# Optimization experiments

Measured on AMD Instinct MI355X. Metric: run time of the kernel, lower is better.

The kernel has to match this reference:

```python
import jax, jax.numpy as jnp
import numpy as np
from jax import lax

B, T, D, H, O, L = 32, 2048, 256, 256, 256, 2


def setup_inputs() -> dict:
    key = jax.random.key(0)
    ks = jax.random.split(key, 16)
    s = 0.05
    inp = {"x": jax.random.normal(ks[0], (B, T, D), dtype=jnp.float32)}
    dims = [D, H]  # input dim of each layer
    for l in range(L):
        inp[f"Wi{l}"] = jax.random.normal(ks[1 + 3 * l], (dims[l], 4 * H), dtype=jnp.float32) * s
        inp[f"Wh{l}"] = jax.random.normal(ks[2 + 3 * l], (H, 4 * H), dtype=jnp.float32) * s
        inp[f"b{l}"] = jnp.zeros((4 * H,), dtype=jnp.float32)
    inp["Wd"] = jax.random.normal(ks[10], (H, O), dtype=jnp.float32) * s
    inp["bd"] = jnp.zeros((O,), dtype=jnp.float32)
    return inp


def _lstm_layer(x, Wi, Wh, b):
    # x: [B, T, Din] -> outputs h over time: [B, T, H]
    Bx = x.shape[0]
    Hh = Wh.shape[0]
    # Precompute input projections for all timesteps (one big GEMM).
    xg = jnp.einsum('btd,dg->tbg', x, Wi)  # time-major [T, B, 4H]

    def step(carry, xg_t):
        c, h = carry
        z = xg_t + h @ Wh + b  # [B, 4H]
        i, f, g, o = jnp.split(z, 4, axis=-1)  # flax gate order: i, f, g, o
        c_new = jax.nn.sigmoid(f) * c + jax.nn.sigmoid(i) * jnp.tanh(g)
        h_new = jax.nn.sigmoid(o) * jnp.tanh(c_new)
        return (c_new, h_new), h_new

    c0 = jnp.zeros((Bx, Hh), dtype=x.dtype)
    h0 = jnp.zeros((Bx, Hh), dtype=x.dtype)
    _, ys = lax.scan(step, (c0, h0), xg)  # ys: [T, B, H]
    return ys.transpose(1, 0, 2)


def reference(x, Wi0, Wh0, b0, Wi1, Wh1, b1, Wd, bd):
    y = _lstm_layer(x, Wi0, Wh0, b0)
    y = _lstm_layer(y, Wi1, Wh1, b1)
    last_hidden = y[:, -1]  # [B, H]
    return last_hidden @ Wd + bd  # [B, O]
```

## Files before the change

kernel.cpp:

```cpp
#include <hip/hip_runtime.h>
#include <stdint.h>

#define TT 2048
#define DD 256
#define GG 1024
#define HWORDS 8192
#define RING0 64
#define RING1 4
#define PROW 1024

typedef __attribute__((ext_vector_type(4))) float f32x4;
typedef __attribute__((ext_vector_type(8))) short s16x8;
typedef __attribute__((ext_vector_type(4))) unsigned u32x4;

static __device__ __forceinline__ unsigned f2bf(float f) {
    union { float f; unsigned u; } v; v.f = f;
    return (v.u + 0x7fffu + ((v.u >> 16) & 1u)) >> 16;
}
static __device__ __forceinline__ float bf2f(unsigned b) {
    union { unsigned u; float f; } v; v.u = b << 16;
    return v.f;
}
static __device__ __forceinline__ float sigm(float x) {
    return 1.0f / (1.0f + __expf(-x));
}
static __device__ __forceinline__ float tanh_f(float x) {
    x = fminf(15.0f, fmaxf(-15.0f, x));
    float e = __expf(2.0f * x);
    return (e - 1.0f) / (e + 1.0f);
}

static __device__ __forceinline__ u32x4 ld16_sys(const unsigned* p) {
    u32x4 r;
    asm volatile("global_load_dwordx4 %0, %1, off sc0 sc1"
                 : "=&v"(r) : "v"(p) : "memory");
    return r;
}
static __device__ __forceinline__ u32x4 ld16(const unsigned* p) {
    u32x4 r;
    asm volatile("global_load_dwordx4 %0, %1, off"
                 : "=&v"(r) : "v"(p) : "memory");
    return r;
}
static __device__ __forceinline__ void st4_sys(unsigned* p, unsigned d) {
    asm volatile("global_store_dword %0, %1, off sc0 sc1" :: "v"(p), "v"(d) : "memory");
}

#define VW(n) do { asm volatile("s_waitcnt vmcnt(" #n ")" ::: "memory"); \
                   __builtin_amdgcn_sched_barrier(0); } while (0)
#define LBAR() do { asm volatile("s_waitcnt lgkmcnt(0)\n\ts_barrier" ::: "memory"); \
                    __builtin_amdgcn_sched_barrier(0); } while (0)

#define KEEP8(a) asm volatile("" :: "v"(a[0]), "v"(a[1]), "v"(a[2]), "v"(a[3]), \
                                    "v"(a[4]), "v"(a[5]), "v"(a[6]), "v"(a[7]))

static __device__ __forceinline__ bool tags_ok4(const u32x4 v[8], unsigned tag) {
    unsigned d = 0;
#pragma unroll
    for (int i = 0; i < 8; ++i)
        d |= (v[i][0] ^ tag) | (v[i][1] ^ tag) | (v[i][2] ^ tag) | (v[i][3] ^ tag);
    return (d & 0xffffu) == 0;
}

__global__ void k_init(unsigned* __restrict__ h0, unsigned* __restrict__ h1) {
    unsigned i = blockIdx.x * 256 + threadIdx.x;
    h0[i] = 0u;
    if (i < RING1 * HWORDS) h1[i] = 0u;
}

__launch_bounds__(256, 1)
__global__ void k_scan(const float* __restrict__ x,
                       const float* __restrict__ Wi0, const float* __restrict__ Wh0,
                       const float* __restrict__ b0,
                       const float* __restrict__ Wi1, const float* __restrict__ Wh1,
                       const float* __restrict__ b1,
                       unsigned* h0w, unsigned* h1w)
{
    const int tid = threadIdx.x;
    const bool isL0 = (blockIdx.x < 32);
    const int w = blockIdx.x & 31;

    const float* Wi = isL0 ? Wi0 : Wi1;
    const float* Wh = isL0 ? Wh0 : Wh1;
    const float* bb = isL0 ? b0 : b1;

    __shared__ __align__(16) unsigned char Ap[32 * PROW];
    __shared__ float zbuf[4 * 32 * 10];

    const int lane = tid & 63;
    const int wid = tid >> 6;
    const int mt = wid & 1;
    const int nt = wid >> 1;

    s16x8 Bf[16];
    {
        const int jloc = lane & 15;
        const int lcol = nt * 16 + jloc;
        const int gate = lcol >> 3;
        const int jj = lcol & 7;
        const int gcol = gate * 256 + w * 8 + jj;
        const int krow = (lane >> 4) * 8;
#pragma unroll
        for (int kf = 0; kf < 16; ++kf) {
            s16x8 a;
#pragma unroll
            for (int j = 0; j < 8; ++j) {
                int k = kf * 32 + krow + j;
                float wv = (k < 256) ? Wi[(size_t)k * GG + gcol] : Wh[(size_t)(k - 256) * GG + gcol];
                a[j] = (short)f2bf(wv);
            }
            Bf[kf] = a;
        }
    }

    const int gm = tid >> 3;
    const int gj = tid & 7;
    const float bi_ = bb[0 * 256 + w * 8 + gj], bf_ = bb[1 * 256 + w * 8 + gj];
    const float bg_ = bb[2 * 256 + w * 8 + gj], bo_ = bb[3 * 256 + w * 8 + gj];

    const int cb = tid & 63;
    const int rq = tid >> 6;

    const unsigned urow = (unsigned)((tid >> 1) & 31);
    const unsigned usw = (urow & 7u) << 4;

    const unsigned arow = (unsigned)(mt * 16 + (lane & 15));
    const unsigned rb = arow * PROW;
    const unsigned asw = (arow & 7u) << 4;

    float cs = 0.f;
    long long budget = 500000;

#define UNP_STORE(A0, A1, A2, A3, BASE, I) do {                                   \
        uint2 pk_;                                                                \
        pk_.x = ((A0) >> 16) | ((A1) & 0xffff0000u);                              \
        pk_.y = ((A2) >> 16) | ((A3) & 0xffff0000u);                              \
        unsigned bcol_ = (unsigned)((I) * 4 + (tid >> 6)) * 16u                   \
                       + (unsigned)(tid & 1) * 8u;                                \
        *(uint2*)(Ap + urow * PROW + (((BASE) + bcol_) ^ usw)) = pk_;             \
    } while (0)

    if (isL0) {
        int known = 0;
        u32x4 xr[8];
#pragma unroll
        for (int i = 0; i < 8; ++i)
            xr[i] = ld16((const unsigned*)(x + (size_t)(i * 4 + rq) * (TT * DD) + cb * 4));
        VW(0);
        u32x4 pA[8] = {}, pB[8] = {};

        for (int c = 0; c < TT; ++c) {
            VW(1);
            KEEP8(pA); KEEP8(pB);
#pragma unroll
            for (int i = 0; i < 8; ++i) {
                unsigned row = (unsigned)(i * 4 + rq);
                uint2 pk;
                pk.x = f2bf(__uint_as_float(xr[i][0])) | (f2bf(__uint_as_float(xr[i][1])) << 16);
                pk.y = f2bf(__uint_as_float(xr[i][2])) | (f2bf(__uint_as_float(xr[i][3])) << 16);
                *(uint2*)(Ap + row * PROW + (((unsigned)(cb * 8)) ^ ((row & 7u) << 4))) = pk;
            }
            const unsigned* s0 = h0w + (size_t)(c & (RING0 - 1)) * HWORDS + tid * 4;
#pragma unroll
            for (int i = 0; i < 8; ++i) pA[i] = ld16_sys(s0 + i * 1024);
            LBAR();

            f32x4 acc = {0.f, 0.f, 0.f, 0.f};
#pragma unroll
            for (int kf = 0; kf < 8; ++kf) {
                unsigned kb = (unsigned)kf * 64u + ((unsigned)(lane >> 4)) * 16u;
                s16x8 a = *(const s16x8*)(Ap + rb + (kb ^ asw));
                acc = __builtin_amdgcn_mfma_f32_16x16x32_bf16(a, Bf[kf], acc, 0, 0, 0);
            }
#pragma unroll
            for (int i = 0; i < 8; ++i) pB[i] = ld16_sys(s0 + i * 1024);
            VW(8);
            bool wA = tags_ok4(pA, (unsigned)c);
            bool ok = wA;
            while (!ok) {
                if (--budget <= 0) break;
                __builtin_amdgcn_s_sleep(1);
#pragma unroll
                for (int i = 0; i < 8; ++i) pA[i] = ld16_sys(s0 + i * 1024);
                VW(8);
                if (tags_ok4(pB, (unsigned)c)) { ok = true; wA = false; break; }
                if (--budget <= 0) break;
                __builtin_amdgcn_s_sleep(1);
#pragma unroll
                for (int i = 0; i < 8; ++i) pB[i] = ld16_sys(s0 + i * 1024);
                VW(8);
                wA = tags_ok4(pA, (unsigned)c);
                ok = wA;
            }
#pragma unroll
            for (int i = 0; i < 8; ++i) {
                unsigned a0 = wA ? pA[i][0] : pB[i][0];
                unsigned a1 = wA ? pA[i][1] : pB[i][1];
                unsigned a2 = wA ? pA[i][2] : pB[i][2];
                unsigned a3 = wA ? pA[i][3] : pB[i][3];
                UNP_STORE(a0, a1, a2, a3, 512u, i);
            }
            if (c + 1 < TT) {
#pragma unroll
                for (int i = 0; i < 8; ++i)
                    xr[i] = ld16((const unsigned*)(x + (size_t)(i * 4 + rq) * (TT * DD)
                                                   + (size_t)(c + 1) * DD + cb * 4));
            }
            LBAR();

#pragma unroll
            for (int kf = 8; kf < 16; ++kf) {
                unsigned kb = (unsigned)kf * 64u + ((unsigned)(lane >> 4)) * 16u;
                s16x8 a = *(const s16x8*)(Ap + rb + (kb ^ asw));
                acc = __builtin_amdgcn_mfma_f32_16x16x32_bf16(a, Bf[kf], acc, 0, 0, 0);
            }
            {
                const int n = nt * 16 + (lane & 15);
                const int g = n >> 3, cl = n & 7;
#pragma unroll
                for (int r = 0; r < 4; ++r)
                    zbuf[g * 320 + (mt * 16 + (lane >> 4) * 4 + r) * 10 + cl] = acc[r];
            }
            LBAR();

            float zi = zbuf[0 * 320 + gm * 10 + gj] + bi_;
            float zf = zbuf[1 * 320 + gm * 10 + gj] + bf_;
            float zg = zbuf[2 * 320 + gm * 10 + gj] + bg_;
            float zo = zbuf[3 * 320 + gm * 10 + gj] + bo_;
            cs = sigm(zf) * cs + sigm(zi) * tanh_f(zg);
            float h = sigm(zo) * tanh_f(cs);

            int T = c - 63;
            if (T > known) {
                const unsigned* trow = h1w + (size_t)(T & (RING1 - 1)) * HWORDS
                                     + (size_t)(lane & 31) * 256;
                for (;;) {
                    u32x4 tv = ld16_sys(trow);
                    VW(0);
                    int m = (int)(tv[0] & 0xffffu);
                    m = min(m, (int)(tv[1] & 0xffffu));
                    m = min(m, (int)(tv[2] & 0xffffu));
                    m = min(m, (int)(tv[3] & 0xffffu));
#pragma unroll
                    for (int off = 32; off; off >>= 1) m = min(m, __shfl_xor(m, off, 64));
                    if (m >= T) { known = m; break; }
                    if (--budget <= 0) break;
                    __builtin_amdgcn_s_sleep(4);
                }
            }
            st4_sys(h0w + (size_t)((c + 1) & (RING0 - 1)) * HWORDS + w * 256 + tid,
                    (f2bf(h) << 16) | (unsigned)(c + 1));
        }
    } else {
        u32x4 ph[8], qA[8] = {}, qB[8] = {};
        {
            const unsigned* sp = h0w + (size_t)1 * HWORDS + tid * 4;
#pragma unroll
            for (int i = 0; i < 8; ++i) ph[i] = ld16_sys(sp + i * 1024);
        }
        for (int c = 0; c < TT; ++c) {
            if (c == 0) { VW(0); } else { VW(1); }
            KEEP8(qA); KEEP8(qB);
            const unsigned* s0 = h0w + (size_t)((c + 1) & (RING0 - 1)) * HWORDS + tid * 4;
            while (!tags_ok4(ph, (unsigned)(c + 1))) {
                if (--budget <= 0) break;
                __builtin_amdgcn_s_sleep(1);
#pragma unroll
                for (int i = 0; i < 8; ++i) ph[i] = ld16_sys(s0 + i * 1024);
                VW(0);
            }
#pragma unroll
            for (int i = 0; i < 8; ++i)
                UNP_STORE(ph[i][0], ph[i][1], ph[i][2], ph[i][3], 0u, i);

            const unsigned* s1 = h1w + (size_t)(c & (RING1 - 1)) * HWORDS + tid * 4;
#pragma unroll
            for (int i = 0; i < 8; ++i) qA[i] = ld16_sys(s1 + i * 1024);
            LBAR();

            f32x4 acc = {0.f, 0.f, 0.f, 0.f};
#pragma unroll
            for (int kf = 0; kf < 8; ++kf) {
                unsigned kb = (unsigned)kf * 64u + ((unsigned)(lane >> 4)) * 16u;
                s16x8 a = *(const s16x8*)(Ap + rb + (kb ^ asw));
                acc = __builtin_amdgcn_mfma_f32_16x16x32_bf16(a, Bf[kf], acc, 0, 0, 0);
            }
#pragma unroll
            for (int i = 0; i < 8; ++i) qB[i] = ld16_sys(s1 + i * 1024);
            VW(8);
            bool wA = tags_ok4(qA, (unsigned)c);
            bool ok = wA;
            while (!ok) {
                if (--budget <= 0) break;
                __builtin_amdgcn_s_sleep(1);
#pragma unroll
                for (int i = 0; i < 8; ++i) qA[i] = ld16_sys(s1 + i * 1024);
                VW(8);
                if (tags_ok4(qB, (unsigned)c)) { ok = true; wA = false; break; }
                if (--budget <= 0) break;
                __builtin_amdgcn_s_sleep(1);
#pragma unroll
                for (int i = 0; i < 8; ++i) qB[i] = ld16_sys(s1 + i * 1024);
                VW(8);
                wA = tags_ok4(qA, (unsigned)c);
                ok = wA;
            }
#pragma unroll
            for (int i = 0; i < 8; ++i) {
                unsigned a0 = wA ? qA[i][0] : qB[i][0];
                unsigned a1 = wA ? qA[i][1] : qB[i][1];
                unsigned a2 = wA ? qA[i][2] : qB[i][2];
                unsigned a3 = wA ? qA[i][3] : qB[i][3];
                UNP_STORE(a0, a1, a2, a3, 512u, i);
            }
            LBAR();

#pragma unroll
            for (int kf = 8; kf < 16; ++kf) {
                unsigned kb = (unsigned)kf * 64u + ((unsigned)(lane >> 4)) * 16u;
                s16x8 a = *(const s16x8*)(Ap + rb + (kb ^ asw));
                acc = __builtin_amdgcn_mfma_f32_16x16x32_bf16(a, Bf[kf], acc, 0, 0, 0);
            }
            {
                const int n = nt * 16 + (lane & 15);
                const int g = n >> 3, cl = n & 7;
#pragma unroll
                for (int r = 0; r < 4; ++r)
                    zbuf[g * 320 + (mt * 16 + (lane >> 4) * 4 + r) * 10 + cl] = acc[r];
            }
            LBAR();

            float zi = zbuf[0 * 320 + gm * 10 + gj] + bi_;
            float zf = zbuf[1 * 320 + gm * 10 + gj] + bf_;
            float zg = zbuf[2 * 320 + gm * 10 + gj] + bg_;
            float zo = zbuf[3 * 320 + gm * 10 + gj] + bo_;
            cs = sigm(zf) * cs + sigm(zi) * tanh_f(zg);
            float h = sigm(zo) * tanh_f(cs);

            if (c + 1 < TT) {
                const unsigned* sn = h0w + (size_t)((c + 2) & (RING0 - 1)) * HWORDS + tid * 4;
#pragma unroll
                for (int i = 0; i < 8; ++i) ph[i] = ld16_sys(sn + i * 1024);
            }
            st4_sys(h1w + (size_t)((c + 1) & (RING1 - 1)) * HWORDS + w * 256 + tid,
                    (f2bf(h) << 16) | (unsigned)(c + 1));
        }
    }
#undef UNP_STORE
}

__global__ void k_dense(const unsigned* __restrict__ h1last,
                        const float* __restrict__ Wd, const float* __restrict__ bd,
                        float* __restrict__ out)
{
    __shared__ float hs[256];
    const int m = blockIdx.x;
    const int o = threadIdx.x;
    hs[o] = bf2f(h1last[(o >> 3) * 256 + m * 8 + (o & 7)] >> 16);
    __syncthreads();
    float acc = bd[o];
#pragma unroll 8
    for (int k = 0; k < 256; ++k)
        acc = fmaf(hs[k], Wd[k * 256 + o], acc);
    out[m * 256 + o] = acc;
}

extern "C" void kernel_launch(void* const* d_in, const int* in_sizes, int n_in,
                              void* d_out, int out_size, void* d_ws, size_t ws_size,
                              hipStream_t stream)
{
    const float* x   = (const float*)d_in[0];
    const float* Wi0 = (const float*)d_in[1];
    const float* Wh0 = (const float*)d_in[2];
    const float* b0  = (const float*)d_in[3];
    const float* Wi1 = (const float*)d_in[4];
    const float* Wh1 = (const float*)d_in[5];
    const float* b1  = (const float*)d_in[6];
    const float* Wd  = (const float*)d_in[7];
    const float* bd  = (const float*)d_in[8];
    float* out = (float*)d_out;

    char* ws = (char*)d_ws;
    unsigned* h0w = (unsigned*)ws;
    unsigned* h1w = (unsigned*)(ws + (size_t)RING0 * HWORDS * 4);

    k_init<<<dim3(RING0 * HWORDS / 256), dim3(256), 0, stream>>>(h0w, h1w);
    k_scan<<<dim3(64), dim3(256), 0, stream>>>(x, Wi0, Wh0, b0, Wi1, Wh1, b1, h0w, h1w);
    k_dense<<<dim3(32), dim3(256), 0, stream>>>(
        h1w + (size_t)(TT & (RING1 - 1)) * HWORDS, Wd, bd, out);
}
```

Baseline: 4.634 ms.

## Restructure recurrent step: issue h polls right after publish, single barrier before MFMA

Replaces the double-buffered pA/pB speculative polling, and the split of the MFMA across two barrier phases, with one poll that is issued right after this block publishes its own h. The next step then only waits and retries before staging both halves into LDS behind a single barrier. The K loop runs as two independent accumulator chains that are summed at the end, which shortens the MFMA dependency chain. The x bf16 conversion is hoisted to the end of the previous step. The risk is that the first poll now often reads stale tags (issued immediately after the store) and needs a sleep-and-retry round trip. It also loses the overlap of the first half of the MFMA with the poll latency.

```diff
diff --git a/kernel.cpp b/kernel.cpp
--- a/kernel.cpp
+++ b/kernel.cpp
@@ -50,9 +50,6 @@
                    __builtin_amdgcn_sched_barrier(0); } while (0)
 #define LBAR() do { asm volatile("s_waitcnt lgkmcnt(0)\n\ts_barrier" ::: "memory"); \
                     __builtin_amdgcn_sched_barrier(0); } while (0)
-
-#define KEEP8(a) asm volatile("" :: "v"(a[0]), "v"(a[1]), "v"(a[2]), "v"(a[3]), \
-                                    "v"(a[4]), "v"(a[5]), "v"(a[6]), "v"(a[7]))
 
 static __device__ __forceinline__ bool tags_ok4(const u32x4 v[8], unsigned tag) {
     unsigned d = 0;
@@ -143,63 +140,41 @@
     if (isL0) {
         int known = 0;
         u32x4 xr[8];
+        uint2 cvt[8];
+        u32x4 pA[8];
 #pragma unroll
         for (int i = 0; i < 8; ++i)
             xr[i] = ld16((const unsigned*)(x + (size_t)(i * 4 + rq) * (TT * DD) + cb * 4));
         VW(0);
-        u32x4 pA[8] = {}, pB[8] = {};
+#pragma unroll
+        for (int i = 0; i < 8; ++i) {
+            cvt[i].x = f2bf(__uint_as_float(xr[i][0])) | (f2bf(__uint_as_float(xr[i][1])) << 16);
+            cvt[i].y = f2bf(__uint_as_float(xr[i][2])) | (f2bf(__uint_as_float(xr[i][3])) << 16);
+        }
+        {
+            const unsigned* s0 = h0w + tid * 4;
+#pragma unroll
+            for (int i = 0; i < 8; ++i) pA[i] = ld16_sys(s0 + i * 1024);
+        }
 
         for (int c = 0; c < TT; ++c) {
-            VW(1);
-            KEEP8(pA); KEEP8(pB);
+            const unsigned* s0 = h0w + (size_t)(c & (RING0 - 1)) * HWORDS + tid * 4;
+            VW(0);
+            while (!tags_ok4(pA, (unsigned)c)) {
+                if (--budget <= 0) break;
+                __builtin_amdgcn_s_sleep(1);
+#pragma unroll
+                for (int i = 0; i < 8; ++i) pA[i] = ld16_sys(s0 + i * 1024);
+                VW(0);
+            }
 #pragma unroll
             for (int i = 0; i < 8; ++i) {
                 unsigned row = (unsigned)(i * 4 + rq);
-                uint2 pk;
-                pk.x = f2bf(__uint_as_float(xr[i][0])) | (f2bf(__uint_as_float(xr[i][1])) << 16);
-                pk.y = f2bf(__uint_as_float(xr[i][2])) | (f2bf(__uint_as_float(xr[i][3])) << 16);
-                *(uint2*)(Ap + row * PROW + (((unsigned)(cb * 8)) ^ ((row & 7u) << 4))) = pk;
-            }
-            const unsigned* s0 = h0w + (size_t)(c & (RING0 - 1)) * HWORDS + tid * 4;
-#pragma unroll
-            for (int i = 0; i < 8; ++i) pA[i] = ld16_sys(s0 + i * 1024);
-            LBAR();
-
-            f32x4 acc = {0.f, 0.f, 0.f, 0.f};
-#pragma unroll
-            for (int kf = 0; kf < 8; ++kf) {
-                unsigned kb = (unsigned)kf * 64u + ((unsigned)(lane >> 4)) * 16u;
-                s16x8 a = *(const s16x8*)(Ap + rb + (kb ^ asw));
-                acc = __builtin_amdgcn_mfma_f32_16x16x32_bf16(a, Bf[kf], acc, 0, 0, 0);
-            }
-#pragma unroll
-            for (int i = 0; i < 8; ++i) pB[i] = ld16_sys(s0 + i * 1024);
-            VW(8);
-            bool wA = tags_ok4(pA, (unsigned)c);
-            bool ok = wA;
-            while (!ok) {
-                if (--budget <= 0) break;
-                __builtin_amdgcn_s_sleep(1);
-#pragma unroll
-                for (int i = 0; i < 8; ++i) pA[i] = ld16_sys(s0 + i * 1024);
-                VW(8);
-                if (tags_ok4(pB, (unsigned)c)) { ok = true; wA = false; break; }
-                if (--budget <= 0) break;
-                __builtin_amdgcn_s_sleep(1);
-#pragma unroll
-                for (int i = 0; i < 8; ++i) pB[i] = ld16_sys(s0 + i * 1024);
-                VW(8);
-                wA = tags_ok4(pA, (unsigned)c);
-                ok = wA;
-            }
-#pragma unroll
-            for (int i = 0; i < 8; ++i) {
-                unsigned a0 = wA ? pA[i][0] : pB[i][0];
-                unsigned a1 = wA ? pA[i][1] : pB[i][1];
-                unsigned a2 = wA ? pA[i][2] : pB[i][2];
-                unsigned a3 = wA ? pA[i][3] : pB[i][3];
-                UNP_STORE(a0, a1, a2, a3, 512u, i);
-            }
+                *(uint2*)(Ap + row * PROW + (((unsigned)(cb * 8)) ^ ((row & 7u) << 4))) = cvt[i];
+            }
+#pragma unroll
+            for (int i = 0; i < 8; ++i)
+                UNP_STORE(pA[i][0], pA[i][1], pA[i][2], pA[i][3], 512u, i);
             if (c + 1 < TT) {
 #pragma unroll
                 for (int i = 0; i < 8; ++i)
@@ -208,13 +183,18 @@
             }
             LBAR();
 
-#pragma unroll
-            for (int kf = 8; kf < 16; ++kf) {
+            f32x4 accA = {0.f, 0.f, 0.f, 0.f};
+            f32x4 accB = {0.f, 0.f, 0.f, 0.f};
+#pragma unroll
+            for (int kf = 0; kf < 8; ++kf) {
                 unsigned kb = (unsigned)kf * 64u + ((unsigned)(lane >> 4)) * 16u;
-                s16x8 a = *(const s16x8*)(Ap + rb + (kb ^ asw));
-                acc = __builtin_amdgcn_mfma_f32_16x16x32_bf16(a, Bf[kf], acc, 0, 0, 0);
+                s16x8 a0 = *(const s16x8*)(Ap + rb + (kb ^ asw));
+                s16x8 a1 = *(const s16x8*)(Ap + rb + ((kb + 512u) ^ asw));
+                accA = __builtin_amdgcn_mfma_f32_16x16x32_bf16(a0, Bf[kf], accA, 0, 0, 0);
+                accB = __builtin_amdgcn_mfma_f32_16x16x32_bf16(a1, Bf[kf + 8], accB, 0, 0, 0);
             }
             {
+                f32x4 acc = accA + accB;
                 const int n = nt * 16 + (lane & 15);
                 const int g = n >> 3, cl = n & 7;
 #pragma unroll
@@ -250,78 +230,66 @@
             }
             st4_sys(h0w + (size_t)((c + 1) & (RING0 - 1)) * HWORDS + w * 256 + tid,
                     (f2bf(h) << 16) | (unsigned)(c + 1));
+            VW(1);
+            if (c + 1 < TT) {
+#pragma unroll
+                for (int i = 0; i < 8; ++i) {
+                    cvt[i].x = f2bf(__uint_as_float(xr[i][0])) | (f2bf(__uint_as_float(xr[i][1])) << 16);
+                    cvt[i].y = f2bf(__uint_as_float(xr[i][2])) | (f2bf(__uint_as_float(xr[i][3])) << 16);
+                }
+                const unsigned* sn = h0w + (size_t)((c + 1) & (RING0 - 1)) * HWORDS + tid * 4;
+#pragma unroll
+                for (int i = 0; i < 8; ++i) pA[i] = ld16_sys(sn + i * 1024);
+            }
         }
     } else {
-        u32x4 ph[8], qA[8] = {}, qB[8] = {};
+        u32x4 ph[8], qA[8];
         {
             const unsigned* sp = h0w + (size_t)1 * HWORDS + tid * 4;
+            const unsigned* sq = h1w + tid * 4;
 #pragma unroll
             for (int i = 0; i < 8; ++i) ph[i] = ld16_sys(sp + i * 1024);
+#pragma unroll
+            for (int i = 0; i < 8; ++i) qA[i] = ld16_sys(sq + i * 1024);
         }
         for (int c = 0; c < TT; ++c) {
-            if (c == 0) { VW(0); } else { VW(1); }
-            KEEP8(qA); KEEP8(qB);
-            const unsigned* s0 = h0w + (size_t)((c + 1) & (RING0 - 1)) * HWORDS + tid * 4;
+            const unsigned* sp = h0w + (size_t)((c + 1) & (RING0 - 1)) * HWORDS + tid * 4;
+            const unsigned* sq = h1w + (size_t)(c & (RING1 - 1)) * HWORDS + tid * 4;
+            VW(0);
             while (!tags_ok4(ph, (unsigned)(c + 1))) {
                 if (--budget <= 0) break;
                 __builtin_amdgcn_s_sleep(1);
 #pragma unroll
-                for (int i = 0; i < 8; ++i) ph[i] = ld16_sys(s0 + i * 1024);
+                for (int i = 0; i < 8; ++i) ph[i] = ld16_sys(sp + i * 1024);
+                VW(0);
+            }
+            while (!tags_ok4(qA, (unsigned)c)) {
+                if (--budget <= 0) break;
+                __builtin_amdgcn_s_sleep(1);
+#pragma unroll
+                for (int i = 0; i < 8; ++i) qA[i] = ld16_sys(sq + i * 1024);
                 VW(0);
             }
 #pragma unroll
             for (int i = 0; i < 8; ++i)
                 UNP_STORE(ph[i][0], ph[i][1], ph[i][2], ph[i][3], 0u, i);
-
-            const unsigned* s1 = h1w + (size_t)(c & (RING1 - 1)) * HWORDS + tid * 4;
-#pragma unroll
-            for (int i = 0; i < 8; ++i) qA[i] = ld16_sys(s1 + i * 1024);
+#pragma unroll
+            for (int i = 0; i < 8; ++i)
+                UNP_STORE(qA[i][0], qA[i][1], qA[i][2], qA[i][3], 512u, i);
             LBAR();
 
-            f32x4 acc = {0.f, 0.f, 0.f, 0.f};
+            f32x4 accA = {0.f, 0.f, 0.f, 0.f};
+            f32x4 accB = {0.f, 0.f, 0.f, 0.f};
 #pragma unroll
             for (int kf = 0; kf < 8; ++kf) {
                 unsigned kb = (unsigned)kf * 64u + ((unsigned)(lane >> 4)) * 16u;
-                s16x8 a = *(const s16x8*)(Ap + rb + (kb ^ asw));
-                acc = __builtin_amdgcn_mfma_f32_16x16x32_bf16(a, Bf[kf], acc, 0, 0, 0);
-            }
-#pragma unroll
-            for (int i = 0; i < 8; ++i) qB[i] = ld16_sys(s1 + i * 1024);
-            VW(8);
-            bool wA = tags_ok4(qA, (unsigned)c);
-            bool ok = wA;
-            while (!ok) {
-                if (--budget <= 0) break;
-                __builtin_amdgcn_s_sleep(1);
-#pragma unroll
-                for (int i = 0; i < 8; ++i) qA[i] = ld16_sys(s1 + i * 1024);
-                VW(8);
-                if (tags_ok4(qB, (unsigned)c)) { ok = true; wA = false; break; }
-                if (--budget <= 0) break;
-                __builtin_amdgcn_s_sleep(1);
-#pragma unroll
-                for (int i = 0; i < 8; ++i) qB[i] = ld16_sys(s1 + i * 1024);
-                VW(8);
-                wA = tags_ok4(qA, (unsigned)c);
-                ok = wA;
-            }
-#pragma unroll
-            for (int i = 0; i < 8; ++i) {
-                unsigned a0 = wA ? qA[i][0] : qB[i][0];
-                unsigned a1 = wA ? qA[i][1] : qB[i][1];
-                unsigned a2 = wA ? qA[i][2] : qB[i][2];
-                unsigned a3 = wA ? qA[i][3] : qB[i][3];
-                UNP_STORE(a0, a1, a2, a3, 512u, i);
-            }
-            LBAR();
-
-#pragma unroll
-            for (int kf = 8; kf < 16; ++kf) {
-                unsigned kb = (unsigned)kf * 64u + ((unsigned)(lane >> 4)) * 16u;
-                s16x8 a = *(const s16x8*)(Ap + rb + (kb ^ asw));
-                acc = __builtin_amdgcn_mfma_f32_16x16x32_bf16(a, Bf[kf], acc, 0, 0, 0);
+                s16x8 a0 = *(const s16x8*)(Ap + rb + (kb ^ asw));
+                s16x8 a1 = *(const s16x8*)(Ap + rb + ((kb + 512u) ^ asw));
+                accA = __builtin_amdgcn_mfma_f32_16x16x32_bf16(a0, Bf[kf], accA, 0, 0, 0);
+                accB = __builtin_amdgcn_mfma_f32_16x16x32_bf16(a1, Bf[kf + 8], accB, 0, 0, 0);
             }
             {
+                f32x4 acc = accA + accB;
                 const int n = nt * 16 + (lane & 15);
                 const int g = n >> 3, cl = n & 7;
 #pragma unroll
@@ -337,13 +305,16 @@
             cs = sigm(zf) * cs + sigm(zi) * tanh_f(zg);
             float h = sigm(zo) * tanh_f(cs);
 
-            if (c + 1 < TT) {
-                const unsigned* sn = h0w + (size_t)((c + 2) & (RING0 - 1)) * HWORDS + tid * 4;
-#pragma unroll
-                for (int i = 0; i < 8; ++i) ph[i] = ld16_sys(sn + i * 1024);
-            }
             st4_sys(h1w + (size_t)((c + 1) & (RING1 - 1)) * HWORDS + w * 256 + tid,
                     (f2bf(h) << 16) | (unsigned)(c + 1));
+            if (c + 1 < TT) {
+                const unsigned* spn = h0w + (size_t)((c + 2) & (RING0 - 1)) * HWORDS + tid * 4;
+                const unsigned* sqn = h1w + (size_t)((c + 1) & (RING1 - 1)) * HWORDS + tid * 4;
+#pragma unroll
+                for (int i = 0; i < 8; ++i) ph[i] = ld16_sys(spn + i * 1024);
+#pragma unroll
+                for (int i = 0; i < 8; ++i) qA[i] = ld16_sys(sqn + i * 1024);
+            }
         }
     }
 #undef UNP_STORE
```

After: 5.983 ms. +29.1%, slower.

## Halve scan workgroups per layer, giving each 16 hidden units

Applied to the files above, without the earlier changes.

Each LSTM layer now runs on 16 workgroups instead of 32, so each workgroup owns 16 hidden columns per gate. It does two MFMA column tiles per step, two cell updates per thread, and publishes a dwordx2 of tagged h values. The h ring layout and k_dense indexing change to match. This roughly halves the number of producers each step must poll for, cutting cross-workgroup sync cost, in exchange for twice the MFMA and gate work per workgroup and more registers for weight fragments.

```diff
diff --git a/kernel.cpp b/kernel.cpp
--- a/kernel.cpp
+++ b/kernel.cpp
@@ -8,6 +8,7 @@
 #define RING0 64
 #define RING1 4
 #define PROW 1024
+#define CREW 16
 
 typedef __attribute__((ext_vector_type(4))) float f32x4;
 typedef __attribute__((ext_vector_type(8))) short s16x8;
@@ -42,8 +43,8 @@
                  : "=&v"(r) : "v"(p) : "memory");
     return r;
 }
-static __device__ __forceinline__ void st4_sys(unsigned* p, unsigned d) {
-    asm volatile("global_store_dword %0, %1, off sc0 sc1" :: "v"(p), "v"(d) : "memory");
+static __device__ __forceinline__ void st8_sys(unsigned* p, uint2 d) {
+    asm volatile("global_store_dwordx2 %0, %1, off sc0 sc1" :: "v"(p), "v"(d) : "memory");
 }
 
 #define VW(n) do { asm volatile("s_waitcnt vmcnt(" #n ")" ::: "memory"); \
@@ -77,28 +78,29 @@
                        unsigned* h0w, unsigned* h1w)
 {
     const int tid = threadIdx.x;
-    const bool isL0 = (blockIdx.x < 32);
-    const int w = blockIdx.x & 31;
+    const bool isL0 = (blockIdx.x < CREW);
+    const int w = blockIdx.x & (CREW - 1);
 
     const float* Wi = isL0 ? Wi0 : Wi1;
     const float* Wh = isL0 ? Wh0 : Wh1;
     const float* bb = isL0 ? b0 : b1;
 
     __shared__ __align__(16) unsigned char Ap[32 * PROW];
-    __shared__ float zbuf[4 * 32 * 10];
+    __shared__ float zbuf[4 * 32 * 18];
 
     const int lane = tid & 63;
     const int wid = tid >> 6;
     const int mt = wid & 1;
     const int nt = wid >> 1;
 
-    s16x8 Bf[16];
-    {
+    s16x8 Bf[2][16];
+#pragma unroll
+    for (int t = 0; t < 2; ++t) {
         const int jloc = lane & 15;
-        const int lcol = nt * 16 + jloc;
-        const int gate = lcol >> 3;
-        const int jj = lcol & 7;
-        const int gcol = gate * 256 + w * 8 + jj;
+        const int lcol = nt * 32 + t * 16 + jloc;
+        const int gate = lcol >> 4;
+        const int jj = lcol & 15;
+        const int gcol = gate * 256 + w * 16 + jj;
         const int krow = (lane >> 4) * 8;
 #pragma unroll
         for (int kf = 0; kf < 16; ++kf) {
@@ -109,35 +111,36 @@
                 float wv = (k < 256) ? Wi[(size_t)k * GG + gcol] : Wh[(size_t)(k - 256) * GG + gcol];
                 a[j] = (short)f2bf(wv);
             }
-            Bf[kf] = a;
+            Bf[t][kf] = a;
         }
     }
 
     const int gm = tid >> 3;
-    const int gj = tid & 7;
-    const float bi_ = bb[0 * 256 + w * 8 + gj], bf_ = bb[1 * 256 + w * 8 + gj];
-    const float bg_ = bb[2 * 256 + w * 8 + gj], bo_ = bb[3 * 256 + w * 8 + gj];
+    const int gj0 = (tid & 7) * 2;
+    const float bi0_ = bb[0 * 256 + w * 16 + gj0], bf0_ = bb[1 * 256 + w * 16 + gj0];
+    const float bg0_ = bb[2 * 256 + w * 16 + gj0], bo0_ = bb[3 * 256 + w * 16 + gj0];
+    const float bi1_ = bb[0 * 256 + w * 16 + gj0 + 1], bf1_ = bb[1 * 256 + w * 16 + gj0 + 1];
+    const float bg1_ = bb[2 * 256 + w * 16 + gj0 + 1], bo1_ = bb[3 * 256 + w * 16 + gj0 + 1];
 
     const int cb = tid & 63;
     const int rq = tid >> 6;
 
-    const unsigned urow = (unsigned)((tid >> 1) & 31);
-    const unsigned usw = (urow & 7u) << 4;
+    const unsigned rp = (unsigned)((tid >> 2) & 31);
+    const unsigned usw = (rp & 7u) << 4;
+    const unsigned cbase2 = (unsigned)((tid >> 7) * 32 + (tid & 3) * 8);
 
     const unsigned arow = (unsigned)(mt * 16 + (lane & 15));
     const unsigned rb = arow * PROW;
     const unsigned asw = (arow & 7u) << 4;
 
-    float cs = 0.f;
+    float cs0 = 0.f, cs1 = 0.f;
     long long budget = 500000;
 
 #define UNP_STORE(A0, A1, A2, A3, BASE, I) do {                                   \
         uint2 pk_;                                                                \
         pk_.x = ((A0) >> 16) | ((A1) & 0xffff0000u);                              \
         pk_.y = ((A2) >> 16) | ((A3) & 0xffff0000u);                              \
-        unsigned bcol_ = (unsigned)((I) * 4 + (tid >> 6)) * 16u                   \
-                       + (unsigned)(tid & 1) * 8u;                                \
-        *(uint2*)(Ap + urow * PROW + (((BASE) + bcol_) ^ usw)) = pk_;             \
+        *(uint2*)(Ap + rp * PROW + (((BASE) + cbase2 + 64u * (unsigned)(I)) ^ usw)) = pk_; \
     } while (0)
 
     if (isL0) {
@@ -165,12 +168,14 @@
             for (int i = 0; i < 8; ++i) pA[i] = ld16_sys(s0 + i * 1024);
             LBAR();
 
-            f32x4 acc = {0.f, 0.f, 0.f, 0.f};
+            f32x4 ac0 = {0.f, 0.f, 0.f, 0.f};
+            f32x4 ac1 = {0.f, 0.f, 0.f, 0.f};
 #pragma unroll
             for (int kf = 0; kf < 8; ++kf) {
                 unsigned kb = (unsigned)kf * 64u + ((unsigned)(lane >> 4)) * 16u;
                 s16x8 a = *(const s16x8*)(Ap + rb + (kb ^ asw));
-                acc = __builtin_amdgcn_mfma_f32_16x16x32_bf16(a, Bf[kf], acc, 0, 0, 0);
+                ac0 = __builtin_amdgcn_mfma_f32_16x16x32_bf16(a, Bf[0][kf], ac0, 0, 0, 0);
+                ac1 = __builtin_amdgcn_mfma_f32_16x16x32_bf16(a, Bf[1][kf], ac1, 0, 0, 0);
             }
 #pragma unroll
             for (int i = 0; i < 8; ++i) pB[i] = ld16_sys(s0 + i * 1024);
@@ -212,28 +217,37 @@
             for (int kf = 8; kf < 16; ++kf) {
                 unsigned kb = (unsigned)kf * 64u + ((unsigned)(lane >> 4)) * 16u;
                 s16x8 a = *(const s16x8*)(Ap + rb + (kb ^ asw));
-                acc = __builtin_amdgcn_mfma_f32_16x16x32_bf16(a, Bf[kf], acc, 0, 0, 0);
-            }
-            {
-                const int n = nt * 16 + (lane & 15);
-                const int g = n >> 3, cl = n & 7;
+                ac0 = __builtin_amdgcn_mfma_f32_16x16x32_bf16(a, Bf[0][kf], ac0, 0, 0, 0);
+                ac1 = __builtin_amdgcn_mfma_f32_16x16x32_bf16(a, Bf[1][kf], ac1, 0, 0, 0);
+            }
+#pragma unroll
+            for (int t = 0; t < 2; ++t) {
+                const int n = nt * 32 + t * 16 + (lane & 15);
+                const int g = n >> 4, cl = n & 15;
+                f32x4 av = t ? ac1 : ac0;
 #pragma unroll
                 for (int r = 0; r < 4; ++r)
-                    zbuf[g * 320 + (mt * 16 + (lane >> 4) * 4 + r) * 10 + cl] = acc[r];
-            }
-            LBAR();
-
-            float zi = zbuf[0 * 320 + gm * 10 + gj] + bi_;
-            float zf = zbuf[1 * 320 + gm * 10 + gj] + bf_;
-            float zg = zbuf[2 * 320 + gm * 10 + gj] + bg_;
-            float zo = zbuf[3 * 320 + gm * 10 + gj] + bo_;
-            cs = sigm(zf) * cs + sigm(zi) * tanh_f(zg);
-            float h = sigm(zo) * tanh_f(cs);
+                    zbuf[g * 576 + (mt * 16 + (lane >> 4) * 4 + r) * 18 + cl] = av[r];
+            }
+            LBAR();
+
+            float zi0 = zbuf[0 * 576 + gm * 18 + gj0] + bi0_;
+            float zf0 = zbuf[1 * 576 + gm * 18 + gj0] + bf0_;
+            float zg0 = zbuf[2 * 576 + gm * 18 + gj0] + bg0_;
+            float zo0 = zbuf[3 * 576 + gm * 18 + gj0] + bo0_;
+            cs0 = sigm(zf0) * cs0 + sigm(zi0) * tanh_f(zg0);
+            float hv0 = sigm(zo0) * tanh_f(cs0);
+            float zi1 = zbuf[0 * 576 + gm * 18 + gj0 + 1] + bi1_;
+            float zf1 = zbuf[1 * 576 + gm * 18 + gj0 + 1] + bf1_;
+            float zg1 = zbuf[2 * 576 + gm * 18 + gj0 + 1] + bg1_;
+            float zo1 = zbuf[3 * 576 + gm * 18 + gj0 + 1] + bo1_;
+            cs1 = sigm(zf1) * cs1 + sigm(zi1) * tanh_f(zg1);
+            float hv1 = sigm(zo1) * tanh_f(cs1);
 
             int T = c - 63;
             if (T > known) {
                 const unsigned* trow = h1w + (size_t)(T & (RING1 - 1)) * HWORDS
-                                     + (size_t)(lane & 31) * 256;
+                                     + (size_t)(lane & 15) * 512;
                 for (;;) {
                     u32x4 tv = ld16_sys(trow);
                     VW(0);
@@ -248,8 +262,10 @@
                     __builtin_amdgcn_s_sleep(4);
                 }
             }
-            st4_sys(h0w + (size_t)((c + 1) & (RING0 - 1)) * HWORDS + w * 256 + tid,
-                    (f2bf(h) << 16) | (unsigned)(c + 1));
+            uint2 pub;
+            pub.x = (f2bf(hv0) << 16) | (unsigned)(c + 1);
+            pub.y = (f2bf(hv1) << 16) | (unsigned)(c + 1);
+            st8_sys(h0w + (size_t)((c + 1) & (RING0 - 1)) * HWORDS + w * 512 + gm * 16 + gj0, pub);
         }
     } else {
         u32x4 ph[8], qA[8] = {}, qB[8] = {};
@@ -278,12 +294,14 @@
             for (int i = 0; i < 8; ++i) qA[i] = ld16_sys(s1 + i * 1024);
             LBAR();
 
-            f32x4 acc = {0.f, 0.f, 0.f, 0.f};
+            f32x4 ac0 = {0.f, 0.f, 0.f, 0.f};
+            f32x4 ac1 = {0.f, 0.f, 0.f, 0.f};
 #pragma unroll
             for (int kf = 0; kf < 8; ++kf) {
                 unsigned kb = (unsigned)kf * 64u + ((unsigned)(lane >> 4)) * 16u;
                 s16x8 a = *(const s16x8*)(Ap + rb + (kb ^ asw));
-                acc = __builtin_amdgcn_mfma_f32_16x16x32_bf16(a, Bf[kf], acc, 0, 0, 0);
+                ac0 = __builtin_amdgcn_mfma_f32_16x16x32_bf16(a, Bf[0][kf], ac0, 0, 0, 0);
+                ac1 = __builtin_amdgcn_mfma_f32_16x16x32_bf16(a, Bf[1][kf], ac1, 0, 0, 0);
             }
 #pragma unroll
             for (int i = 0; i < 8; ++i) qB[i] = ld16_sys(s1 + i * 1024);
@@ -319,31 +337,42 @@
             for (int kf = 8; kf < 16; ++kf) {
                 unsigned kb = (unsigned)kf * 64u + ((unsigned)(lane >> 4)) * 16u;
                 s16x8 a = *(const s16x8*)(Ap + rb + (kb ^ asw));
-                acc = __builtin_amdgcn_mfma_f32_16x16x32_bf16(a, Bf[kf], acc, 0, 0, 0);
-            }
-            {
-                const int n = nt * 16 + (lane & 15);
-                const int g = n >> 3, cl = n & 7;
+                ac0 = __builtin_amdgcn_mfma_f32_16x16x32_bf16(a, Bf[0][kf], ac0, 0, 0, 0);
+                ac1 = __builtin_amdgcn_mfma_f32_16x16x32_bf16(a, Bf[1][kf], ac1, 0, 0, 0);
+            }
+#pragma unroll
+            for (int t = 0; t < 2; ++t) {
+                const int n = nt * 32 + t * 16 + (lane & 15);
+                const int g = n >> 4, cl = n & 15;
+                f32x4 av = t ? ac1 : ac0;
 #pragma unroll
                 for (int r = 0; r < 4; ++r)
-                    zbuf[g * 320 + (mt * 16 + (lane >> 4) * 4 + r) * 10 + cl] = acc[r];
-            }
-            LBAR();
-
-            float zi = zbuf[0 * 320 + gm * 10 + gj] + bi_;
-            float zf = zbuf[1 * 320 + gm * 10 + gj] + bf_;
-            float zg = zbuf[2 * 320 + gm * 10 + gj] + bg_;
-            float zo = zbuf[3 * 320 + gm * 10 + gj] + bo_;
-            cs = sigm(zf) * cs + sigm(zi) * tanh_f(zg);
-            float h = sigm(zo) * tanh_f(cs);
+                    zbuf[g * 576 + (mt * 16 + (lane >> 4) * 4 + r) * 18 + cl] = av[r];
+            }
+            LBAR();
+
+            float zi0 = zbuf[0 * 576 + gm * 18 + gj0] + bi0_;
+            float zf0 = zbuf[1 * 576 + gm * 18 + gj0] + bf0_;
+            float zg0 = zbuf[2 * 576 + gm * 18 + gj0] + bg0_;
+            float zo0 = zbuf[3 * 576 + gm * 18 + gj0] + bo0_;
+            cs0 = sigm(zf0) * cs0 + sigm(zi0) * tanh_f(zg0);
+            float hv0 = sigm(zo0) * tanh_f(cs0);
+            float zi1 = zbuf[0 * 576 + gm * 18 + gj0 + 1] + bi1_;
+            float zf1 = zbuf[1 * 576 + gm * 18 + gj0 + 1] + bf1_;
+            float zg1 = zbuf[2 * 576 + gm * 18 + gj0 + 1] + bg1_;
+            float zo1 = zbuf[3 * 576 + gm * 18 + gj0 + 1] + bo1_;
+            cs1 = sigm(zf1) * cs1 + sigm(zi1) * tanh_f(zg1);
+            float hv1 = sigm(zo1) * tanh_f(cs1);
 
             if (c + 1 < TT) {
                 const unsigned* sn = h0w + (size_t)((c + 2) & (RING0 - 1)) * HWORDS + tid * 4;
 #pragma unroll
                 for (int i = 0; i < 8; ++i) ph[i] = ld16_sys(sn + i * 1024);
             }
-            st4_sys(h1w + (size_t)((c + 1) & (RING1 - 1)) * HWORDS + w * 256 + tid,
-                    (f2bf(h) << 16) | (unsigned)(c + 1));
+            uint2 pub;
+            pub.x = (f2bf(hv0) << 16) | (unsigned)(c + 1);
+            pub.y = (f2bf(hv1) << 16) | (unsigned)(c + 1);
+            st8_sys(h1w + (size_t)((c + 1) & (RING1 - 1)) * HWORDS + w * 512 + gm * 16 + gj0, pub);
         }
     }
 #undef UNP_STORE
@@ -356,7 +385,7 @@
     __shared__ float hs[256];
     const int m = blockIdx.x;
     const int o = threadIdx.x;
-    hs[o] = bf2f(h1last[(o >> 3) * 256 + m * 8 + (o & 7)] >> 16);
+    hs[o] = bf2f(h1last[(o >> 4) * 512 + m * 16 + (o & 15)] >> 16);
     __syncthreads();
     float acc = bd[o];
 #pragma unroll 8
@@ -385,7 +414,7 @@
     unsigned* h1w = (unsigned*)(ws + (size_t)RING0 * HWORDS * 4);
 
     k_init<<<dim3(RING0 * HWORDS / 256), dim3(256), 0, stream>>>(h0w, h1w);
-    k_scan<<<dim3(64), dim3(256), 0, stream>>>(x, Wi0, Wh0, b0, Wi1, Wh1, b1, h0w, h1w);
+    k_scan<<<dim3(2 * CREW), dim3(256), 0, stream>>>(x, Wi0, Wh0, b0, Wi1, Wh1, b1, h0w, h1w);
     k_dense<<<dim3(32), dim3(256), 0, stream>>>(
         h1w + (size_t)(TT & (RING1 - 1)) * HWORDS, Wd, bd, out);
 }
```

Measured after the change: 5.729 ms. 1.24x slower.
